# Kernel tuning notes

Measured on AMD Instinct MI355X. Metric: run time of the kernel, lower is better.

Reference implementation:

```python
import jax, jax.numpy as jnp
import numpy as np

B, N, F_IN, F_OUT, H = 4, 2048, 128, 256, 4
HD = F_OUT // H


def setup_inputs() -> dict:
    key = jax.random.key(0)
    k1, k2, k3, k4, k5 = jax.random.split(key, 5)
    x = jax.random.normal(k1, (B, N, F_IN), dtype=jnp.float32)
    adj = jax.random.randint(k2, (B, N, N), 0, 2, dtype=jnp.int32)
    # xavier-ish scaled params
    W = jax.random.normal(k3, (F_OUT, F_IN), dtype=jnp.float32) * float(np.sqrt(2.0 / (F_IN + F_OUT)))
    a_l = jax.random.normal(k4, (H, HD), dtype=jnp.float32) * float(np.sqrt(2.0 / (H * HD + 1)))
    a_r = jax.random.normal(k5, (H, HD), dtype=jnp.float32) * float(np.sqrt(2.0 / (H * HD + 1)))
    return {"x": x, "adj": adj, "W": W, "a_l": a_l, "a_r": a_r}


def reference(x, adj, W, a_l, a_r):
    Bb, Nn, _ = x.shape
    h = jnp.einsum('bnf,of->bno', x, W).reshape(Bb, Nn, H, HD)   # [B,N,H,HD]
    e_l = jnp.einsum('bnhd,hd->bnh', h, a_l)                      # [B,N,H]
    e_r = jnp.einsum('bnhd,hd->bnh', h, a_r)                      # [B,N,H]
    e = e_l[:, :, None, :] + e_r[:, None, :, :]                   # [B,N(i),N(j),H]
    e = jax.nn.leaky_relu(e, negative_slope=0.2)
    e = jnp.where(adj[..., None] == 0, -jnp.inf, e)
    alpha = jax.nn.softmax(e, axis=2)                             # softmax over neighbors j
    out = jnp.einsum('bijh,bjhd->bihd', alpha, h)                 # [B,N,H,HD]
    return out.reshape(Bb, Nn, F_OUT)
```

## Files before the change

### kernel.cpp

```cpp
#include <hip/hip_runtime.h>
#include <stdint.h>

#define BB 4
#define NN 2048
#define F_IN 128
#define F_OUT 256
#define NH 4
#define HD 64

typedef float f32x4 __attribute__((ext_vector_type(4)));
typedef float f32x2 __attribute__((ext_vector_type(2)));
typedef short s16x8 __attribute__((ext_vector_type(8)));
typedef int i32x4 __attribute__((ext_vector_type(4)));
typedef unsigned long long u64;
typedef unsigned short u16;

#define LOG2E 1.4426950408889634f

__device__ __forceinline__ u16 f32_to_bf16_rtn(float f) {
    union { float f; uint32_t u; } v; v.f = f;
    uint32_t u = v.u;
    u += 0x7fffu + ((u >> 16) & 1u);
    return (u16)(u >> 16);
}

__device__ __forceinline__ float exp2_fast(float x) {
#if __has_builtin(__builtin_amdgcn_exp2f)
    return __builtin_amdgcn_exp2f(x);
#else
    return exp2f(x);
#endif
}

__device__ __forceinline__ int sbfe1(uint32_t v, int k) {
#if __has_builtin(__builtin_amdgcn_sbfe)
    return __builtin_amdgcn_sbfe((int)v, k, 1);
#else
    return ((int32_t)(v << (31 - k))) >> 31;
#endif
}

__global__ __launch_bounds__(256) void k01(
    const int* __restrict__ adj, const float* __restrict__ x,
    const float* __restrict__ W, const float* __restrict__ a_l,
    const float* __restrict__ a_r, uint32_t* __restrict__ abits32,
    u16* __restrict__ hB, float* __restrict__ el, f32x2* __restrict__ er12)
{
    const int t = threadIdx.x;

    __shared__ __align__(16) float red[4 * 64 * 20];
    float (*xs)[F_IN] = (float(*)[F_IN])red;

    const int bid = blockIdx.x;
    if ((bid % 5) != 4) {
        const int pack_id = bid - (bid + 1) / 5;
        const int row = (pack_id << 2) | (t >> 6);
        const int wd = t & 63;
        const int* wp = adj + (size_t)row * NN + wd * 32;
        i32x4 v[8];
#pragma unroll
        for (int u = 0; u < 8; ++u) v[u] = *(const i32x4*)(wp + 4 * u);
        uint32_t word = 0;
#pragma unroll
        for (int u = 0; u < 8; ++u) {
#pragma unroll
            for (int e = 0; e < 4; ++e)
                word |= (uint32_t)(v[u][e] != 0) << (4 * u + e);
        }
        abits32[(size_t)row * 64 + wd] = word;
        return;
    }

    const int proj_id = bid / 5;
    const int b = proj_id >> 7;
    const int n0 = (proj_id & 127) * 16;

    {
        const f32x4* src = (const f32x4*)(x + ((size_t)b * NN + n0) * F_IN);
        f32x4* dst = (f32x4*)&xs[0][0];
        dst[t] = src[t];
        dst[t + 256] = src[t + 256];
    }
    __syncthreads();

    float acc[16];
#pragma unroll
    for (int n = 0; n < 16; ++n) acc[n] = 0.f;

    const float* wrow = W + (size_t)t * F_IN;
#pragma unroll 2
    for (int k0 = 0; k0 < F_IN; k0 += 8) {
        f32x4 w0 = *(const f32x4*)(wrow + k0);
        f32x4 w1 = *(const f32x4*)(wrow + k0 + 4);
#pragma unroll
        for (int n = 0; n < 16; ++n) {
            f32x4 xa = *(const f32x4*)&xs[n][k0];
            f32x4 xb = *(const f32x4*)&xs[n][k0 + 4];
            float s = acc[n];
            s = fmaf(xa[0], w0[0], s); s = fmaf(xa[1], w0[1], s);
            s = fmaf(xa[2], w0[2], s); s = fmaf(xa[3], w0[3], s);
            s = fmaf(xb[0], w1[0], s); s = fmaf(xb[1], w1[1], s);
            s = fmaf(xb[2], w1[2], s); s = fmaf(xb[3], w1[3], s);
            acc[n] = s;
        }
    }
    __syncthreads();

    const int w = t >> 6, lane = t & 63;
    const float al = a_l[t];
    const float ar = a_r[t];
    const int n_ = lane & 15, og = lane >> 4;
    float sl, sr;
    {
        float* rp = &red[((size_t)w * 64 + lane) * 20];
#pragma unroll
        for (int q = 0; q < 4; ++q) {
            f32x4 v;
#pragma unroll
            for (int e = 0; e < 4; ++e) v[e] = acc[q * 4 + e] * al;
            *(f32x4*)(rp + q * 4) = v;
        }
    }
    __syncthreads();
    {
        float s = 0.f;
#pragma unroll
        for (int oo = 0; oo < 16; ++oo)
            s += red[((size_t)w * 64 + og + 4 * oo) * 20 + n_];
        s += __shfl_xor(s, 16, 64); s += __shfl_xor(s, 32, 64);
        sl = s;
    }
    __syncthreads();
    {
        float* rp = &red[((size_t)w * 64 + lane) * 20];
#pragma unroll
        for (int q = 0; q < 4; ++q) {
            f32x4 v;
#pragma unroll
            for (int e = 0; e < 4; ++e) v[e] = acc[q * 4 + e] * ar;
            *(f32x4*)(rp + q * 4) = v;
        }
    }
    __syncthreads();
    {
        float s = 0.f;
#pragma unroll
        for (int oo = 0; oo < 16; ++oo)
            s += red[((size_t)w * 64 + og + 4 * oo) * 20 + n_];
        s += __shfl_xor(s, 16, 64); s += __shfl_xor(s, 32, 64);
        sr = s;
    }
    if (lane < 16) {
        el[((size_t)b * NH + w) * NN + n0 + lane] = sl * LOG2E;
        float sre = sr * LOG2E;
        f32x2 v2; v2[0] = exp2_fast(sre); v2[1] = exp2_fast(0.2f * sre);
        er12[((size_t)b * NH + w) * NN + n0 + lane] = v2;
    }

    const int dcol = t & 15, cb = (t >> 4) & 3;
    const int jt32 = n0 >> 5;
    const int lb = dcol + ((n0 >> 3) & 2) * 16;
    u16* hb = hB + ((((size_t)b * 64 + jt32) * 4 + w) * 4 + cb) * 512 + (size_t)lb * 8;
    s16x8 pk0, pk1;
#pragma unroll
    for (int n = 0; n < 8; ++n) pk0[n] = (short)f32_to_bf16_rtn(acc[n]);
#pragma unroll
    for (int n = 0; n < 8; ++n) pk1[n] = (short)f32_to_bf16_rtn(acc[n + 8]);
    *(s16x8*)hb         = pk0;
    *(s16x8*)(hb + 128) = pk1;
}

#define MSTRIDE 68

__global__ __launch_bounds__(256, 3) void k2_attn(
    const uint32_t* __restrict__ abits32, const u16* __restrict__ hB,
    const float* __restrict__ el, const f32x2* __restrict__ er12,
    float* __restrict__ out)
{
    __shared__ __align__(16) char smem[33792];
    float*    er_lds   = (float*)smem;
    uint32_t* mask_lds = (uint32_t*)(smem + 16384);
    float*    racc     = (float*)smem;

    const int t = threadIdx.x;
    const int jq = t >> 6, l = t & 63;
    const int o = blockIdx.x;
    const int kblk = o >> 3;
    const int bw = (o & 7) + 8 * (kblk & 1);
    const int b = bw >> 2;
    const int w = bw & 3;
    const int i0 = (kblk >> 1) * 32;
    const int r = l & 15;
    const int kb = l >> 4;
    const int ks = kb * 8;
    const int irow0 = i0 + r, irow1 = irow0 + 16;

    {
        const f32x4* gsrc = (const f32x4*)(er12 + (size_t)(b * NH + w) * NN);
        f32x4* edst = (f32x4*)er_lds;
#pragma unroll
        for (int p = 0; p < 4; ++p) edst[t + p * 256] = gsrc[t + p * 256];
        const i32x4* msrc = (const i32x4*)(abits32 + ((size_t)b * NN + i0) * 64);
        i32x4 mv0 = msrc[t * 2];
        i32x4 mv1 = msrc[t * 2 + 1];
        const int mrow = t >> 3, mc = (t & 7) * 8;
        *(i32x4*)&mask_lds[mrow * MSTRIDE + mc]     = mv0;
        *(i32x4*)&mask_lds[mrow * MSTRIDE + mc + 4] = mv1;
    }

    const u16* hbp = hB + ((((size_t)b * 64 + jq * 16) * 4 + w) * 4) * 512 + (size_t)l * 8;
    const float eli0 = el[((size_t)b * NH + w) * NN + irow0];
    const float eli1 = el[((size_t)b * NH + w) * NN + irow1];
    const float E1i0 = exp2_fast(eli0), E2i0 = exp2_fast(0.2f * eli0);
    const float E1i1 = exp2_fast(eli1), E2i1 = exp2_fast(0.2f * eli1);

    f32x4 a00 = {0.f,0.f,0.f,0.f}, a01 = a00, a02 = a00, a03 = a00, as0 = a00;
    f32x4 a10 = a00, a11 = a00, a12 = a00, a13 = a00, as1 = a00;
    s16x8 ones;
#pragma unroll
    for (int k = 0; k < 8; ++k) ones[k] = (short)0x3F80;

    s16x8 b0c = *(const s16x8*)(hbp + 0 * 512);
    s16x8 b1c = *(const s16x8*)(hbp + 1 * 512);
    s16x8 b2c = *(const s16x8*)(hbp + 2 * 512);
    s16x8 b3c = *(const s16x8*)(hbp + 3 * 512);
    __syncthreads();

#define MFMA_BF16 __builtin_amdgcn_mfma_f32_16x16x32_bf16
#define BODY(IT, PF)                                                          \
    {                                                                         \
        const int itv = (IT);                                                 \
        const int jb2 = (jq * 512 + itv * 32 + ks) * 2;                       \
        f32x4 e0 = *(const f32x4*)(er_lds + jb2);                             \
        f32x4 e1 = *(const f32x4*)(er_lds + jb2 + 4);                         \
        f32x4 e2 = *(const f32x4*)(er_lds + jb2 + 8);                         \
        f32x4 e3 = *(const f32x4*)(er_lds + jb2 + 12);                        \
        uint32_t w2a = mask_lds[r * MSTRIDE + jq * 16 + itv] >> ks;           \
        uint32_t w2b = mask_lds[(16 + r) * MSTRIDE + jq * 16 + itv] >> ks;    \
        s16x8 b0n, b1n, b2n, b3n;                                             \
        if (PF) {                                                             \
            const u16* hp_ = hbp + (size_t)(itv + 1) * 8192;                  \
            b0n = *(const s16x8*)(hp_ + 0 * 512);                             \
            b1n = *(const s16x8*)(hp_ + 1 * 512);                             \
            b2n = *(const s16x8*)(hp_ + 2 * 512);                             \
            b3n = *(const s16x8*)(hp_ + 3 * 512);                             \
        }                                                                     \
        __builtin_amdgcn_sched_barrier(0);                                    \
        union { s16x8 v; uint32_t u[4]; } afa, afb;                           \
        _Pragma("unroll")                                                     \
        for (int kk = 0; kk < 4; ++kk) {                                      \
            f32x4 ev = (kk == 0) ? e0 : ((kk == 1) ? e1 : ((kk == 2) ? e2 : e3)); \
            float t00 = E1i0 * ev[0], m00 = E2i0 * ev[1];                     \
            float t01 = E1i0 * ev[2], m01 = E2i0 * ev[3];                     \
            float t10 = E1i1 * ev[0], m10 = E2i1 * ev[1];                     \
            float t11 = E1i1 * ev[2], m11 = E2i1 * ev[3];                     \
            float p00 = fmaxf(t00, m00);           \
            float p01 = fmaxf(t01, m01);                                      \
            float p10 = fmaxf(t10, m10);                                      \
            float p11 = fmaxf(t11, m11);                                      \
            union { float f; uint32_t u; } c00, c01, c10, c11;                \
            c00.f = p00; c01.f = p01; c10.f = p10; c11.f = p11;               \
            uint32_t q00 = c00.u & (uint32_t)sbfe1(w2a, 2 * kk);              \
            uint32_t q01 = c01.u & (uint32_t)sbfe1(w2a, 2 * kk + 1);          \
            uint32_t q10 = c10.u & (uint32_t)sbfe1(w2b, 2 * kk);              \
            uint32_t q11 = c11.u & (uint32_t)sbfe1(w2b, 2 * kk + 1);          \
            afa.u[kk] = __builtin_amdgcn_perm(q01, q00, 0x07060302);          \
            afb.u[kk] = __builtin_amdgcn_perm(q11, q10, 0x07060302);          \
        }                                                                     \
        a00 = MFMA_BF16(afa.v, b0c, a00, 0, 0, 0);                            \
        a01 = MFMA_BF16(afa.v, b1c, a01, 0, 0, 0);                            \
        a02 = MFMA_BF16(afa.v, b2c, a02, 0, 0, 0);                            \
        a03 = MFMA_BF16(afa.v, b3c, a03, 0, 0, 0);                            \
        as0 = MFMA_BF16(afa.v, ones, as0, 0, 0, 0);                           \
        a10 = MFMA_BF16(afb.v, b0c, a10, 0, 0, 0);                            \
        a11 = MFMA_BF16(afb.v, b1c, a11, 0, 0, 0);                            \
        a12 = MFMA_BF16(afb.v, b2c, a12, 0, 0, 0);                            \
        a13 = MFMA_BF16(afb.v, b3c, a13, 0, 0, 0);                            \
        as1 = MFMA_BF16(afb.v, ones, as1, 0, 0, 0);                           \
        if (PF) { b0c = b0n; b1c = b1n; b2c = b2n; b3c = b3n; }               \
    }

    for (int g = 0; g < 3; ++g) {
#pragma unroll
        for (int s = 0; s < 4; ++s) BODY(g * 4 + s, 1);
    }
    BODY(12, 1); BODY(13, 1); BODY(14, 1); BODY(15, 0);

    __syncthreads();
    if (jq > 0) {
        float* p = &racc[((jq - 1) * 64 + l) * 44];
        *(f32x4*)(p +  0) = a00; *(f32x4*)(p +  4) = a01;
        *(f32x4*)(p +  8) = a02; *(f32x4*)(p + 12) = a03;
        *(f32x4*)(p + 16) = as0;
        *(f32x4*)(p + 20) = a10; *(f32x4*)(p + 24) = a11;
        *(f32x4*)(p + 28) = a12; *(f32x4*)(p + 32) = a13;
        *(f32x4*)(p + 36) = as1;
    }
    __syncthreads();
    if (jq == 0) {
#pragma unroll
        for (int s = 0; s < 3; ++s) {
            const float* p = &racc[(s * 64 + l) * 44];
            a00 += *(const f32x4*)(p +  0); a01 += *(const f32x4*)(p +  4);
            a02 += *(const f32x4*)(p +  8); a03 += *(const f32x4*)(p + 12);
            as0 += *(const f32x4*)(p + 16);
            a10 += *(const f32x4*)(p + 20); a11 += *(const f32x4*)(p + 24);
            a12 += *(const f32x4*)(p + 28); a13 += *(const f32x4*)(p + 32);
            as1 += *(const f32x4*)(p + 36);
        }

        float* op = out + ((size_t)b * NN + i0) * F_OUT + w * HD;
#pragma unroll
        for (int q = 0; q < 4; ++q) {
            const int row0 = kb * 4 + q;
            float inv0 = 1.0f / as0[q];
            __builtin_nontemporal_store(a00[q] * inv0, &op[(size_t)row0 * F_OUT +  0 + r]);
            __builtin_nontemporal_store(a01[q] * inv0, &op[(size_t)row0 * F_OUT + 16 + r]);
            __builtin_nontemporal_store(a02[q] * inv0, &op[(size_t)row0 * F_OUT + 32 + r]);
            __builtin_nontemporal_store(a03[q] * inv0, &op[(size_t)row0 * F_OUT + 48 + r]);
            const int row1 = 16 + kb * 4 + q;
            float inv1 = 1.0f / as1[q];
            __builtin_nontemporal_store(a10[q] * inv1, &op[(size_t)row1 * F_OUT +  0 + r]);
            __builtin_nontemporal_store(a11[q] * inv1, &op[(size_t)row1 * F_OUT + 16 + r]);
            __builtin_nontemporal_store(a12[q] * inv1, &op[(size_t)row1 * F_OUT + 32 + r]);
            __builtin_nontemporal_store(a13[q] * inv1, &op[(size_t)row1 * F_OUT + 48 + r]);
        }
    }
}

extern "C" void kernel_launch(void* const* d_in, const int* in_sizes, int n_in,
                              void* d_out, int out_size, void* d_ws, size_t ws_size,
                              hipStream_t stream) {
    const float* x   = (const float*)d_in[0];
    const int*   adj = (const int*)d_in[1];
    const float* W   = (const float*)d_in[2];
    const float* a_l = (const float*)d_in[3];
    const float* a_r = (const float*)d_in[4];
    float* out = (float*)d_out;

    char* ws = (char*)d_ws;
    u16*      hB      = (u16*)ws;
    uint32_t* abits32 = (uint32_t*)(ws + (size_t)BB * F_OUT * NN * 2);
    float*    el      = (float*)(ws + (size_t)BB * F_OUT * NN * 2 + (size_t)BB * NN * 256);
    f32x2*    er12    = (f32x2*)(el + (size_t)BB * NH * NN);

    k01<<<2560, 256, 0, stream>>>(adj, x, W, a_l, a_r, abits32, hB, el, er12);
    k2_attn<<<BB * NH * (NN / 32), 256, 0, stream>>>(abits32, hB, el, er12, out);
}
```

Baseline: 56.10 us.

## Use bf16 MFMA for projection and coalesce adjacency bit-packing with shuffles

The projection in k01 moves from scalar fp32 FMAs to bf16 MFMA (16x16x32), converting x and W to bf16 on the fly. The attention logits el/er are now reduced with cross-lane shuffles instead of several LDS round trips and barriers, and h is staged through LDS to keep the packed hB store layout. The adjacency packing loads coalesced i32x4 strides and assembles the bit words with xor shuffles. The projection now rounds its inputs to bf16 where it was fp32 before, which lowers precision of h and of the attention logits.

```diff
diff --git a/kernel.cpp b/kernel.cpp
--- a/kernel.cpp
+++ b/kernel.cpp
@@ -12,6 +12,7 @@
 typedef float f32x2 __attribute__((ext_vector_type(2)));
 typedef short s16x8 __attribute__((ext_vector_type(8)));
 typedef int i32x4 __attribute__((ext_vector_type(4)));
+typedef unsigned int u32x2 __attribute__((ext_vector_type(2)));
 typedef unsigned long long u64;
 typedef unsigned short u16;
 
@@ -39,6 +40,17 @@
     return ((int32_t)(v << (31 - k))) >> 31;
 #endif
 }
+
+__device__ __forceinline__ s16x8 pack_bf16x8(f32x4 a, f32x4 b) {
+    union { s16x8 v; u16 h[8]; } pk;
+    pk.h[0] = f32_to_bf16_rtn(a[0]); pk.h[1] = f32_to_bf16_rtn(a[1]);
+    pk.h[2] = f32_to_bf16_rtn(a[2]); pk.h[3] = f32_to_bf16_rtn(a[3]);
+    pk.h[4] = f32_to_bf16_rtn(b[0]); pk.h[5] = f32_to_bf16_rtn(b[1]);
+    pk.h[6] = f32_to_bf16_rtn(b[2]); pk.h[7] = f32_to_bf16_rtn(b[3]);
+    return pk.v;
+}
+
+#define MFMA_BF16 __builtin_amdgcn_mfma_f32_16x16x32_bf16
 
 __global__ __launch_bounds__(256) void k01(
     const int* __restrict__ adj, const float* __restrict__ x,
@@ -47,127 +59,129 @@
     u16* __restrict__ hB, float* __restrict__ el, f32x2* __restrict__ er12)
 {
     const int t = threadIdx.x;
-
-    __shared__ __align__(16) float red[4 * 64 * 20];
-    float (*xs)[F_IN] = (float(*)[F_IN])red;
+    __shared__ __align__(16) u16 psmem[2048 + 256 * 24];
 
     const int bid = blockIdx.x;
     if ((bid % 5) != 4) {
         const int pack_id = bid - (bid + 1) / 5;
         const int row = (pack_id << 2) | (t >> 6);
-        const int wd = t & 63;
-        const int* wp = adj + (size_t)row * NN + wd * 32;
+        const int l = t & 63;
+        const i32x4* rowp = (const i32x4*)(adj + (size_t)row * NN) + l;
         i32x4 v[8];
 #pragma unroll
-        for (int u = 0; u < 8; ++u) v[u] = *(const i32x4*)(wp + 4 * u);
-        uint32_t word = 0;
+        for (int u = 0; u < 8; ++u) v[u] = rowp[u * 64];
+        const int sh = (l & 7) * 4;
+        uint32_t w[8];
 #pragma unroll
         for (int u = 0; u < 8; ++u) {
-#pragma unroll
-            for (int e = 0; e < 4; ++e)
-                word |= (uint32_t)(v[u][e] != 0) << (4 * u + e);
-        }
-        abits32[(size_t)row * 64 + wd] = word;
+            uint32_t nib = (uint32_t)(v[u][0] != 0)
+                         | ((uint32_t)(v[u][1] != 0) << 1)
+                         | ((uint32_t)(v[u][2] != 0) << 2)
+                         | ((uint32_t)(v[u][3] != 0) << 3);
+            uint32_t xv = nib << sh;
+            xv |= __shfl_xor(xv, 1, 64);
+            xv |= __shfl_xor(xv, 2, 64);
+            xv |= __shfl_xor(xv, 4, 64);
+            w[u] = xv;
+        }
+        abits32[(size_t)row * 64 + (l & 7) * 8 + (l >> 3)] = w[l & 7];
         return;
     }
+
+    u16* xA    = psmem;
+    u16* h_lds = psmem + 2048;
 
     const int proj_id = bid / 5;
     const int b = proj_id >> 7;
     const int n0 = (proj_id & 127) * 16;
+    const int w = t >> 6, l = t & 63;
 
     {
-        const f32x4* src = (const f32x4*)(x + ((size_t)b * NN + n0) * F_IN);
-        f32x4* dst = (f32x4*)&xs[0][0];
-        dst[t] = src[t];
-        dst[t + 256] = src[t + 256];
-    }
-    __syncthreads();
-
-    float acc[16];
-#pragma unroll
-    for (int n = 0; n < 16; ++n) acc[n] = 0.f;
-
-    const float* wrow = W + (size_t)t * F_IN;
-#pragma unroll 2
-    for (int k0 = 0; k0 < F_IN; k0 += 8) {
-        f32x4 w0 = *(const f32x4*)(wrow + k0);
-        f32x4 w1 = *(const f32x4*)(wrow + k0 + 4);
-#pragma unroll
-        for (int n = 0; n < 16; ++n) {
-            f32x4 xa = *(const f32x4*)&xs[n][k0];
-            f32x4 xb = *(const f32x4*)&xs[n][k0 + 4];
-            float s = acc[n];
-            s = fmaf(xa[0], w0[0], s); s = fmaf(xa[1], w0[1], s);
-            s = fmaf(xa[2], w0[2], s); s = fmaf(xa[3], w0[3], s);
-            s = fmaf(xb[0], w1[0], s); s = fmaf(xb[1], w1[1], s);
-            s = fmaf(xb[2], w1[2], s); s = fmaf(xb[3], w1[3], s);
-            acc[n] = s;
-        }
-    }
-    __syncthreads();
-
-    const int w = t >> 6, lane = t & 63;
-    const float al = a_l[t];
-    const float ar = a_r[t];
-    const int n_ = lane & 15, og = lane >> 4;
-    float sl, sr;
+        const int n = t >> 4, kg = t & 15;
+        const float* xp = x + ((size_t)b * NN + n0 + n) * F_IN + kg * 8;
+        f32x4 xa = *(const f32x4*)xp;
+        f32x4 xb = *(const f32x4*)(xp + 4);
+        *(s16x8*)(xA + (size_t)((kg >> 2) * 64 + n + 16 * (kg & 3)) * 8) =
+            pack_bf16x8(xa, xb);
+    }
+    __syncthreads();
+
+    s16x8 A0 = *(const s16x8*)(xA + (size_t)(0 * 64 + l) * 8);
+    s16x8 A1 = *(const s16x8*)(xA + (size_t)(1 * 64 + l) * 8);
+    s16x8 A2 = *(const s16x8*)(xA + (size_t)(2 * 64 + l) * 8);
+    s16x8 A3 = *(const s16x8*)(xA + (size_t)(3 * 64 + l) * 8);
+
+    f32x4 acc[4];
+#pragma unroll
+    for (int ot = 0; ot < 4; ++ot) acc[ot] = (f32x4){0.f, 0.f, 0.f, 0.f};
+
+#pragma unroll
+    for (int ot = 0; ot < 4; ++ot) {
+        const float* wbase = W + ((size_t)(w * 64 + ot * 16 + (l & 15))) * F_IN + (l >> 4) * 8;
+#pragma unroll
+        for (int kt = 0; kt < 4; ++kt) {
+            const float* wp = wbase + kt * 32;
+            f32x4 wa = *(const f32x4*)wp;
+            f32x4 wb = *(const f32x4*)(wp + 4);
+            s16x8 bw = pack_bf16x8(wa, wb);
+            s16x8 Af = (kt == 0) ? A0 : ((kt == 1) ? A1 : ((kt == 2) ? A2 : A3));
+            acc[ot] = MFMA_BF16(Af, bw, acc[ot], 0, 0, 0);
+        }
+    }
+
     {
-        float* rp = &red[((size_t)w * 64 + lane) * 20];
+        float alv[4], arv[4];
+#pragma unroll
+        for (int ot = 0; ot < 4; ++ot) {
+            alv[ot] = a_l[w * 64 + ot * 16 + (l & 15)];
+            arv[ot] = a_r[w * 64 + ot * 16 + (l & 15)];
+        }
+        float vL[4], vR[4];
 #pragma unroll
         for (int q = 0; q < 4; ++q) {
-            f32x4 v;
-#pragma unroll
-            for (int e = 0; e < 4; ++e) v[e] = acc[q * 4 + e] * al;
-            *(f32x4*)(rp + q * 4) = v;
-        }
+            vL[q] = acc[0][q] * alv[0] + acc[1][q] * alv[1]
+                  + acc[2][q] * alv[2] + acc[3][q] * alv[3];
+            vR[q] = acc[0][q] * arv[0] + acc[1][q] * arv[1]
+                  + acc[2][q] * arv[2] + acc[3][q] * arv[3];
+        }
+#pragma unroll
+        for (int off = 1; off < 16; off <<= 1) {
+#pragma unroll
+            for (int q = 0; q < 4; ++q) {
+                vL[q] += __shfl_xor(vL[q], off, 64);
+                vR[q] += __shfl_xor(vR[q], off, 64);
+            }
+        }
+        if ((l & 15) == 0) {
+#pragma unroll
+            for (int q = 0; q < 4; ++q) {
+                const int n = n0 + (l >> 4) * 4 + q;
+                el[((size_t)b * NH + w) * NN + n] = vL[q] * LOG2E;
+                float sre = vR[q] * LOG2E;
+                f32x2 v2; v2[0] = exp2_fast(sre); v2[1] = exp2_fast(0.2f * sre);
+                er12[((size_t)b * NH + w) * NN + n] = v2;
+            }
+        }
+    }
+
+#pragma unroll
+    for (int ot = 0; ot < 4; ++ot) {
+        union { u32x2 d; u16 h[4]; } pq;
+#pragma unroll
+        for (int q = 0; q < 4; ++q) pq.h[q] = f32_to_bf16_rtn(acc[ot][q]);
+        *(u32x2*)(h_lds + (size_t)(w * 64 + ot * 16 + (l & 15)) * 24 + (l >> 4) * 4) = pq.d;
     }
     __syncthreads();
     {
-        float s = 0.f;
-#pragma unroll
-        for (int oo = 0; oo < 16; ++oo)
-            s += red[((size_t)w * 64 + og + 4 * oo) * 20 + n_];
-        s += __shfl_xor(s, 16, 64); s += __shfl_xor(s, 32, 64);
-        sl = s;
-    }
-    __syncthreads();
-    {
-        float* rp = &red[((size_t)w * 64 + lane) * 20];
-#pragma unroll
-        for (int q = 0; q < 4; ++q) {
-            f32x4 v;
-#pragma unroll
-            for (int e = 0; e < 4; ++e) v[e] = acc[q * 4 + e] * ar;
-            *(f32x4*)(rp + q * 4) = v;
-        }
-    }
-    __syncthreads();
-    {
-        float s = 0.f;
-#pragma unroll
-        for (int oo = 0; oo < 16; ++oo)
-            s += red[((size_t)w * 64 + og + 4 * oo) * 20 + n_];
-        s += __shfl_xor(s, 16, 64); s += __shfl_xor(s, 32, 64);
-        sr = s;
-    }
-    if (lane < 16) {
-        el[((size_t)b * NH + w) * NN + n0 + lane] = sl * LOG2E;
-        float sre = sr * LOG2E;
-        f32x2 v2; v2[0] = exp2_fast(sre); v2[1] = exp2_fast(0.2f * sre);
-        er12[((size_t)b * NH + w) * NN + n0 + lane] = v2;
-    }
-
-    const int dcol = t & 15, cb = (t >> 4) & 3;
-    const int jt32 = n0 >> 5;
-    const int lb = dcol + ((n0 >> 3) & 2) * 16;
-    u16* hb = hB + ((((size_t)b * 64 + jt32) * 4 + w) * 4 + cb) * 512 + (size_t)lb * 8;
-    s16x8 pk0, pk1;
-#pragma unroll
-    for (int n = 0; n < 8; ++n) pk0[n] = (short)f32_to_bf16_rtn(acc[n]);
-#pragma unroll
-    for (int n = 0; n < 8; ++n) pk1[n] = (short)f32_to_bf16_rtn(acc[n + 8]);
-    *(s16x8*)hb         = pk0;
-    *(s16x8*)(hb + 128) = pk1;
+        const int dcol = t & 15, cb = (t >> 4) & 3, hw = t >> 6;
+        const u16* src = h_lds + (size_t)(hw * 64 + cb * 16 + dcol) * 24;
+        s16x8 g0 = *(const s16x8*)src;
+        s16x8 g1 = *(const s16x8*)(src + 8);
+        const int j8 = (n0 >> 3) & 2;
+        u16* hb = hB + ((((size_t)b * 64 + (n0 >> 5)) * 4 + hw) * 4 + cb) * 512;
+        *(s16x8*)(hb + (size_t)(dcol + 16 * j8) * 8)       = g0;
+        *(s16x8*)(hb + (size_t)(dcol + 16 * (j8 + 1)) * 8) = g1;
+    }
 }
 
 #define MSTRIDE 68
@@ -226,7 +240,6 @@
     s16x8 b3c = *(const s16x8*)(hbp + 3 * 512);
     __syncthreads();
 
-#define MFMA_BF16 __builtin_amdgcn_mfma_f32_16x16x32_bf16
 #define BODY(IT, PF)                                                          \
     {                                                                         \
         const int itv = (IT);                                                 \
```

After: 45.08 us. -19.6%, faster.
